# Performance work log

Measured on AMD Instinct MI355X. Metric: run time of the kernel, lower is better.

## Reference

```python
import jax, jax.numpy as jnp
import numpy as np

N_NODES = 100_000
N_EDGES = 1_600_000
N_GRAPHS = 512
HID = 64
NUM_CLASSES = 100
VOCAB = 3100
ID_OFFSET = 1500
BN_EPS = 1e-5


def setup_inputs() -> dict:
    key = jax.random.key(0)
    ks = jax.random.split(key, 8)
    node_ids = jax.random.randint(ks[0], (N_NODES,), 0, 1600)
    edge_src = jax.random.randint(ks[1], (N_EDGES,), 0, N_NODES)
    edge_dst = jax.random.randint(ks[2], (N_EDGES,), 0, N_NODES)
    graph_ids = jnp.sort(jax.random.randint(ks[3], (N_NODES,), 0, N_GRAPHS))
    emb = jax.random.normal(ks[4], (VOCAB, HID), dtype=jnp.float32) * 0.02
    # 3 GIN layers x 3 MLP linear layers, all 64->64 since embedding_dim == hidden
    Ws = jax.random.normal(ks[5], (3, 3, HID, HID), dtype=jnp.float32) * 0.05
    bs = jnp.zeros((3, 3, HID), dtype=jnp.float32)
    bn_gamma = jnp.ones((3, HID), dtype=jnp.float32)
    bn_beta = jnp.zeros((3, HID), dtype=jnp.float32)
    eps = jnp.zeros((3,), dtype=jnp.float32)  # learn_eps=True, init 0
    W_out = jax.random.normal(ks[6], (3 * HID, NUM_CLASSES), dtype=jnp.float32) * 0.05
    b_out = jnp.zeros((NUM_CLASSES,), dtype=jnp.float32)
    return {"node_ids": node_ids, "edge_src": edge_src, "edge_dst": edge_dst,
            "graph_ids": graph_ids, "emb": emb, "Ws": Ws, "bs": bs,
            "bn_gamma": bn_gamma, "bn_beta": bn_beta, "eps": eps,
            "W_out": W_out, "b_out": b_out}


def reference(node_ids, edge_src, edge_dst, graph_ids, emb, Ws, bs,
              bn_gamma, bn_beta, eps, W_out, b_out):
    n = node_ids.shape[0]
    h = emb[node_ids + ID_OFFSET]  # [N, HID]
    pooled = []
    for l in range(3):  # GIN layers (fixed small count)
        # GINConv, sum aggregator: (1+eps)*h + sum over in-edges of h[src]
        agg = jax.ops.segment_sum(h[edge_src], edge_dst, num_segments=n)
        x = (1.0 + eps[l]) * h + agg
        for m in range(3):
            x = jax.nn.relu(x @ Ws[l, m] + bs[l, m])
        mean = x.mean(axis=0)
        var = x.var(axis=0)  # biased var, as torch BN uses for normalization
        x = (x - mean) * jax.lax.rsqrt(var + BN_EPS) * bn_gamma[l] + bn_beta[l]
        h = x
        # dgl.sum_nodes: per-graph segment sum
        pooled.append(jax.ops.segment_sum(h, graph_ids, num_segments=N_GRAPHS))
    graph_features = jnp.concatenate(pooled, axis=-1)  # [G, 3*HID]
    return graph_features @ W_out + b_out  # [G, NUM_CLASSES]
```

## Files before the change

### kernel.cpp

```cpp
#include <hip/hip_runtime.h>

#define N_NODES 100000
#define N_EDGES 1600000
#define N_GRAPHS 512
#define HID 64
#define NUM_CLASSES 100
#define ID_OFFSET 1500
#define BN_EPS 1e-5f
#define CAP 64
#define NBKT 256
#define BSHIFT 9
#define NUSED ((N_NODES + 511) >> 9)
#define BCAP 10240
#define CBLK 98
#define CHUNK 16384
#define WPBLK 5
#define EMBBLK ((N_NODES * 32 + 1023) / 1024)
#define DUMMY_ROW 100000

typedef __attribute__((ext_vector_type(8))) short short8;
typedef __attribute__((ext_vector_type(4))) float floatx4;

__device__ __forceinline__ float b2f(unsigned short u) {
    return __builtin_bit_cast(float, ((unsigned)u) << 16);
}
__device__ __forceinline__ unsigned short f2b(float f) {
    unsigned x = __builtin_bit_cast(unsigned, f);
    x += 0x7FFFu + ((x >> 16) & 1u);
    return (unsigned short)(x >> 16);
}

#define XSH(row, qq) ((((((row) >> 4) << 7) + ((qq) << 4) + (((row) & 15) ^ (qq))) * 8))


__global__ __launch_bounds__(1024) void prep_kernel(const int* __restrict__ src,
                                                    const int* __restrict__ dst,
                                                    int* __restrict__ cursor,
                                                    int* __restrict__ rec,
                                                    const float* __restrict__ Ws,
                                                    unsigned short* __restrict__ whi,
                                                    unsigned short* __restrict__ wlo,
                                                    const int* __restrict__ node_ids,
                                                    const int* __restrict__ gid,
                                                    const float* __restrict__ emb,
                                                    unsigned short* __restrict__ h,
                                                    unsigned short* __restrict__ xin,
                                                    int* __restrict__ gs,
                                                    int* __restrict__ ge) {
    __shared__ int hist[NBKT];
    __shared__ int base_s[NBKT];
    int t = threadIdx.x;
    int blk = blockIdx.x;

    if (blk < CBLK) {
        if (blk == 0 && t < 32) {
            ((unsigned*)(h + (size_t)DUMMY_ROW * 64))[t] = 0u;
            ((unsigned*)(xin + (size_t)DUMMY_ROW * 64))[t] = 0u;
        }
        if (t < NBKT) hist[t] = 0;
        __syncthreads();
        int cb = blk * CHUNK;
        int d_[16], s_[16];
#pragma unroll
        for (int k = 0; k < 16; ++k) {
            int i = cb + k * 1024 + t;
            d_[k] = (i < N_EDGES) ? dst[i] : -1;
            s_[k] = (i < N_EDGES) ? src[i] : 0;
            if (d_[k] >= 0) atomicAdd(&hist[((unsigned)d_[k] >> BSHIFT) & (NBKT - 1)], 1);
        }
        __syncthreads();
        if (t < NBKT) base_s[t] = (hist[t] > 0) ? atomicAdd(&cursor[t], hist[t]) : 0;
        __syncthreads();
        if (t < NBKT) hist[t] = 0;
        __syncthreads();
#pragma unroll
        for (int k = 0; k < 16; ++k) {
            if (d_[k] >= 0) {
                unsigned d = (unsigned)d_[k];
                int b = (d >> BSHIFT) & (NBKT - 1);
                int p = atomicAdd(&hist[b], 1);
                int g = base_s[b] + p;
                if ((unsigned)g < BCAP)
                    rec[b * BCAP + g] = ((int)(d & 511) << 17) | (s_[k] & 0x1FFFF);
            }
        }
    } else if (blk < CBLK + WPBLK) {
        int G = (blk - CBLK) * 1024 + t;
        if (G < 3 * 1536) {
            int l = G / 1536, Gp = G % 1536;
            int mm = Gp >> 9, rem = Gp & 511;
            int kq = rem >> 6, n = rem & 63;
            const float* Wp = Ws + l * 12288 + mm * 4096 + (kq * 8) * 64 + n;
            unsigned short uh[8], ul[8];
#pragma unroll
            for (int j = 0; j < 8; ++j) {
                float w = Wp[j * 64];
                unsigned short hi = f2b(w);
                uh[j] = hi;
                ul[j] = f2b(w - b2f(hi));
            }
            size_t off = (size_t)l * 12288 + (mm << 12) + XSH(n, kq);
            *(short8*)&whi[off] = *(short8*)uh;
            *(short8*)&wlo[off] = *(short8*)ul;
        }
    } else {
        int idx = (blk - CBLK - WPBLK) * 1024 + t;
        if (idx < N_NODES * 32) {
            int n = idx >> 5, cp = idx & 31;
            const float2 e = *(const float2*)(emb + (((size_t)(node_ids[n] + ID_OFFSET)) << 6) + cp * 2);
            unsigned v = (unsigned)f2b(e.x) | ((unsigned)f2b(e.y) << 16);
            ((unsigned*)h)[n * 32 + cp] = v;
            if (cp == 0) {
                int g = gid[n] & (N_GRAPHS - 1);
                if (n == 0 || (gid[n - 1] & (N_GRAPHS - 1)) != g) gs[g] = n;
                if (n == N_NODES - 1 || (gid[n + 1] & (N_GRAPHS - 1)) != g) ge[g] = n + 1;
            }
        }
    }
}


__global__ __launch_bounds__(1024) void fill_kernel(const int* __restrict__ rec,
                                                    const int* __restrict__ cursor,
                                                    int* __restrict__ cnt,
                                                    int* __restrict__ srcs) {
    __shared__ int lcnt[512];
    int t = threadIdx.x;
    int b = blockIdx.x;
    if (t < 512) lcnt[t] = 0;
    __syncthreads();
    int nb = cursor[b];
    if (nb < 0) nb = 0;
    if (nb > BCAP) nb = BCAP;
    const int* seg = rec + b * BCAP;
    for (int i = t; i < nb; i += 1024) {
        unsigned r = (unsigned)seg[i];
        int dl = (int)((r >> 17) & 511);
        int s = (int)(r & 0x1FFFF);
        int node = (b << BSHIFT) + dl;
        int p = atomicAdd(&lcnt[dl], 1);
        if (p < CAP && node < N_NODES) srcs[(node << 6) + p] = s;
    }
    __syncthreads();
    if (t < 512) {
        int node = (b << BSHIFT) + t;
        if (node < N_NODES) {
            int deg = lcnt[t];
            cnt[node] = deg;
            int degc = deg > CAP ? CAP : deg;
            int degp = (degc + 15) & ~15;
            if (degp < 16) degp = 16;
            for (int p = degc; p < degp; ++p) srcs[(node << 6) + p] = DUMMY_ROW;
        }
    }
}


__global__ __launch_bounds__(256, 4) void fused_kernel(const unsigned short* __restrict__ x,
                                                       unsigned short* __restrict__ xo,
                                                       const int* __restrict__ cnt,
                                                       const int* __restrict__ srcs,
                                                       const float* __restrict__ eps, int l,
                                                       float* __restrict__ stats,
                                                       const float* __restrict__ gamma,
                                                       const float* __restrict__ beta,
                                                       const unsigned short* __restrict__ whi,
                                                       const unsigned short* __restrict__ wlo,
                                                       const float* __restrict__ bs,
                                                       const int* __restrict__ graph_ids,
                                                       float* __restrict__ pooled, int last) {
    __shared__ __align__(16) unsigned short xs[64 * 64];
    __shared__ int garr[64];
    __shared__ float ssum[256], sqq[256];
    int t = threadIdx.x;
    int nodebase = blockIdx.x * 64;
    int lane = t & 63, w = t >> 6;
    int half = lane >> 5, cl = lane & 31;
    const unsigned* __restrict__ xu = (const unsigned*)x;

    if (lane < 16) {
        int n = nodebase + w * 16 + lane;
        garr[w * 16 + lane] = (n < N_NODES) ? (graph_ids[n] & (N_GRAPHS - 1)) : -1;
    }

    float scale = 1.0f + eps[l];
    float a0f = 1.0f, a1f = 1.0f, b0f = 0.0f, b1f = 0.0f;
    if (l > 0) {
        int lp = l - 1;
        float2 sm = *(const float2*)&stats[lp * 128 + 2 * cl];
        float2 sq = *(const float2*)&stats[lp * 128 + 64 + 2 * cl];
        float2 gm = *(const float2*)&gamma[lp * 64 + 2 * cl];
        float2 bt = *(const float2*)&beta[lp * 64 + 2 * cl];
        float mean0 = sm.x * (1.0f / N_NODES);
        float var0 = sq.x * (1.0f / N_NODES) - mean0 * mean0;
        float r0 = rsqrtf(var0 + BN_EPS);
        a0f = gm.x * r0;
        b0f = bt.x - mean0 * a0f;
        float mean1 = sm.y * (1.0f / N_NODES);
        float var1 = sq.y * (1.0f / N_NODES) - mean1 * mean1;
        float r1 = rsqrtf(var1 + BN_EPS);
        a1f = gm.y * r1;
        b1f = bt.y - mean1 * a1f;
    }

    int wb = __builtin_amdgcn_readfirstlane(nodebase + w * 16);

    for (int g4 = 0; g4 < 4; ++g4) {
        int nb = wb + g4 * 4;
        int deg[4], degp[4];
        const int* row[4];
#pragma unroll
        for (int n = 0; n < 4; ++n) {
            int d = (nb + n < N_NODES) ? cnt[nb + n] : 0;
            int dc = d < 0 ? 0 : (d > CAP ? CAP : d);
            deg[n] = dc;
            int dp = (dc + 15) & ~15;
            degp[n] = dp < 16 ? 16 : dp;
            row[n] = srcs + ((size_t)(nb + n) << 6);
        }
        int cmax = degp[0];
        cmax = degp[1] > cmax ? degp[1] : cmax;
        cmax = degp[2] > cmax ? degp[2] : cmax;
        cmax = degp[3] > cmax ? degp[3] : cmax;

        unsigned us[4];
#pragma unroll
        for (int n = 0; n < 4; ++n) us[n] = xu[(size_t)(nb + n) * 32 + cl];

        float A0[4] = {0.f, 0.f, 0.f, 0.f}, A1[4] = {0.f, 0.f, 0.f, 0.f};
        float B0[4] = {0.f, 0.f, 0.f, 0.f}, B1[4] = {0.f, 0.f, 0.f, 0.f};

        {
            unsigned uv[4][8];
#pragma unroll
            for (int n = 0; n < 4; ++n)
#pragma unroll
                for (int k = 0; k < 8; ++k) {
                    int ia = row[n][2 * k] & 0x1FFFF;
                    int ib = row[n][2 * k + 1] & 0x1FFFF;
                    int idx = half ? ib : ia;
                    uv[n][k] = xu[(size_t)idx * 32 + cl];
                }
#pragma unroll
            for (int n = 0; n < 4; ++n)
#pragma unroll
                for (int k = 0; k < 8; ++k) {
                    float lo = b2f((unsigned short)(uv[n][k] & 0xFFFF));
                    float hi = b2f((unsigned short)(uv[n][k] >> 16));
                    if (k & 1) { B0[n] += lo; B1[n] += hi; }
                    else       { A0[n] += lo; A1[n] += hi; }
                }
        }
        for (int c = 16; c < cmax; c += 16) {
            unsigned uc[4][8];
#pragma unroll
            for (int n = 0; n < 4; ++n)
                if (c < degp[n])
#pragma unroll
                    for (int k = 0; k < 8; ++k) {
                        int ia = row[n][c + 2 * k] & 0x1FFFF;
                        int ib = row[n][c + 2 * k + 1] & 0x1FFFF;
                        int idx = half ? ib : ia;
                        uc[n][k] = xu[(size_t)idx * 32 + cl];
                    }
#pragma unroll
            for (int n = 0; n < 4; ++n)
                if (c < degp[n])
#pragma unroll
                    for (int k = 0; k < 8; ++k) {
                        float lo = b2f((unsigned short)(uc[n][k] & 0xFFFF));
                        float hi = b2f((unsigned short)(uc[n][k] >> 16));
                        if (k & 1) { B0[n] += lo; B1[n] += hi; }
                        else       { A0[n] += lo; A1[n] += hi; }
                    }
        }

#pragma unroll
        for (int n = 0; n < 4; ++n) {
            float S0 = A0[n] + B0[n];
            float S1 = A1[n] + B1[n];
            S0 += __shfl_xor(S0, 32);
            S1 += __shfl_xor(S1, 32);
            if (half == 0) {
                float selflo = b2f((unsigned short)(us[n] & 0xFFFF));
                float selfhi = b2f((unsigned short)(us[n] >> 16));
                float db = scale + (float)deg[n];
                float v0 = fmaf(a0f, fmaf(scale, selflo, S0), db * b0f);
                float v1 = fmaf(a1f, fmaf(scale, selfhi, S1), db * b1f);
                int r = w * 16 + g4 * 4 + n;
                int col = 2 * cl;
                *(unsigned*)&xs[XSH(r, col >> 3) + (col & 7)] =
                    (unsigned)f2b(v0) | ((unsigned)f2b(v1) << 16);
            }
        }
    }

    int m = lane & 15, q = lane >> 4;
    const float* bb = bs + l * 3 * 64;
    const unsigned short* whil = whi + (size_t)l * 12288;
    const unsigned short* wlol = wlo + (size_t)l * 12288;
    for (int mm = 0; mm < 3; ++mm) {
        short8 bl[2][4];
#pragma unroll
        for (int kc = 0; kc < 2; ++kc)
#pragma unroll
            for (int tj = 0; tj < 4; ++tj)
                bl[kc][tj] = *(const short8*)&wlol[(mm << 12) + XSH(tj * 16 + m, kc * 4 + q)];
        short8 a[2];
#pragma unroll
        for (int kc = 0; kc < 2; ++kc)
            a[kc] = *(const short8*)&xs[XSH(w * 16 + m, kc * 4 + q)];

        floatx4 acc[4];
#pragma unroll
        for (int tj = 0; tj < 4; ++tj) {
            float bv = bb[mm * 64 + tj * 16 + m];
            acc[tj] = (floatx4){bv, bv, bv, bv};
        }
#pragma unroll
        for (int kc = 0; kc < 2; ++kc) {
            short8 bh[4];
#pragma unroll
            for (int tj = 0; tj < 4; ++tj)
                bh[tj] = *(const short8*)&whil[(mm << 12) + XSH(tj * 16 + m, kc * 4 + q)];
#pragma unroll
            for (int tj = 0; tj < 4; ++tj)
                acc[tj] = __builtin_amdgcn_mfma_f32_16x16x32_bf16(a[kc], bh[tj], acc[tj], 0, 0, 0);
        }
#pragma unroll
        for (int kc = 0; kc < 2; ++kc)
#pragma unroll
            for (int tj = 0; tj < 4; ++tj)
                acc[tj] = __builtin_amdgcn_mfma_f32_16x16x32_bf16(a[kc], bl[kc][tj], acc[tj], 0, 0, 0);
#pragma unroll
        for (int tj = 0; tj < 4; ++tj) {
            int col = tj * 16 + m;
#pragma unroll
            for (int r = 0; r < 4; ++r) {
                int row = w * 16 + q * 4 + r;
                float v = acc[tj][r];
                xs[XSH(row, col >> 3) + (col & 7)] = f2b(v > 0.f ? v : 0.f);
            }
        }
    }

    if (!last) {
        unsigned* xou = (unsigned*)xo;
#pragma unroll
        for (int it = 0; it < 8; ++it) {
            int row = w * 16 + (lane >> 5) + it * 2;
            int cp = lane & 31;
            int col = cp * 2;
            unsigned val = *(const unsigned*)&xs[XSH(row, col >> 3) + (col & 7)];
            int node = nodebase + row;
            if (node < N_NODES) xou[(size_t)node * 32 + cp] = val;
        }
    }
    {
        int c = lane;
        float s = 0.f, q2 = 0.f, acc2 = 0.f;
        int cur = -1;
        for (int k = 0; k < 16; ++k) {
            int row = w * 16 + k;
            int g = garr[row];
            if (g >= 0) {
                float v = b2f(xs[XSH(row, c >> 3) + (c & 7)]);
                s += v;
                q2 += v * v;
                if (g != cur) {
                    if (cur >= 0) atomicAdd(&pooled[cur * 192 + l * 64 + c], acc2);
                    acc2 = 0.f;
                    cur = g;
                }
                acc2 += v;
            }
        }
        if (cur >= 0) atomicAdd(&pooled[cur * 192 + l * 64 + c], acc2);
        ssum[t] = s;
        sqq[t] = q2;
    }
    __syncthreads();
    if (t < 64) {
        float S = ssum[t] + ssum[t + 64] + ssum[t + 128] + ssum[t + 192];
        float Q = sqq[t] + sqq[t + 64] + sqq[t + 128] + sqq[t + 192];
        atomicAdd(&stats[l * 128 + t], S);
        atomicAdd(&stats[l * 128 + 64 + t], Q);
    }
}


__global__ __launch_bounds__(256) void out_kernel(const float* __restrict__ pooled,
                                                  const float* __restrict__ stats,
                                                  const float* __restrict__ gamma,
                                                  const float* __restrict__ beta,
                                                  const int* __restrict__ gs,
                                                  const int* __restrict__ ge,
                                                  const float* __restrict__ Wo,
                                                  const float* __restrict__ bo,
                                                  float* __restrict__ out) {
    __shared__ float sab[384];
    int t = threadIdx.x;
    if (t < 192) {
        int l2 = t / 64, c = t & 63;
        float mean = stats[l2 * 128 + c] * (1.0f / N_NODES);
        float var = stats[l2 * 128 + 64 + c] * (1.0f / N_NODES) - mean * mean;
        float rstd = rsqrtf(var + BN_EPS);
        float a = gamma[l2 * 64 + c] * rstd;
        sab[l2 * 128 + c] = a;
        sab[l2 * 128 + 64 + c] = beta[l2 * 64 + c] - mean * a;
    }
    __syncthreads();
    int idx = blockIdx.x * blockDim.x + t;
    if (idx < N_GRAPHS * NUM_CLASSES) {
        int g = idx / NUM_CLASSES, k = idx % NUM_CLASSES;
        float cg = (float)(ge[g] - gs[g]);
        float acc = bo[k];
        for (int l2 = 0; l2 < 3; ++l2)
            for (int c = 0; c < 64; ++c) {
                float gf = fmaf(sab[l2 * 128 + c], pooled[g * 192 + l2 * 64 + c],
                                sab[l2 * 128 + 64 + c] * cg);
                acc = fmaf(gf, Wo[(l2 * 64 + c) * NUM_CLASSES + k], acc);
            }
        out[idx] = acc;
    }
}

extern "C" void kernel_launch(void* const* d_in, const int* in_sizes, int n_in,
                              void* d_out, int out_size, void* d_ws, size_t ws_size,
                              hipStream_t stream) {
    const int*   node_ids  = (const int*)d_in[0];
    const int*   edge_src  = (const int*)d_in[1];
    const int*   edge_dst  = (const int*)d_in[2];
    const int*   graph_ids = (const int*)d_in[3];
    const float* emb       = (const float*)d_in[4];
    const float* Ws        = (const float*)d_in[5];
    const float* bs        = (const float*)d_in[6];
    const float* gamma     = (const float*)d_in[7];
    const float* beta      = (const float*)d_in[8];
    const float* eps       = (const float*)d_in[9];
    const float* W_out     = (const float*)d_in[10];
    const float* b_out     = (const float*)d_in[11];
    float* out = (float*)d_out;

    unsigned short* h    = (unsigned short*)d_ws;
    unsigned short* xin  = h + 6400000 + 8192;
    unsigned short* whi  = xin + 6400000 + 8192;
    unsigned short* wlo  = whi + 36864;
    int*   srcs   = (int*)(wlo + 36864);
    int*   rec    = srcs + 6400000;
    float* pooled = (float*)(rec + NUSED * BCAP);
    float* stats  = pooled + 98304;
    int*   cnt    = (int*)(stats + 384);
    int*   gs     = cnt + 100000;
    int*   ge     = gs + 512;
    int*   cursor = ge + 512;

    hipMemsetAsync(pooled, 0,
                   (size_t)(98304 + 384 + 100000 + 512 + 512 + 256) * 4, stream);

    prep_kernel<<<CBLK + WPBLK + EMBBLK, 1024, 0, stream>>>(
        edge_src, edge_dst, cursor, rec, Ws, whi, wlo,
        node_ids, graph_ids, emb, h, xin, gs, ge);
    fill_kernel<<<NUSED, 1024, 0, stream>>>(rec, cursor, cnt, srcs);

    const int FUSE_BLK = (N_NODES + 63) / 64;
    for (int l = 0; l < 3; ++l) {
        const unsigned short* X = (l % 2 == 0) ? h : xin;
        unsigned short* A = (l % 2 == 0) ? xin : h;
        fused_kernel<<<FUSE_BLK, 256, 0, stream>>>(
            X, A, cnt, srcs, eps, l, stats, gamma, beta,
            whi, wlo, bs, graph_ids, pooled, l == 2);
    }

    out_kernel<<<(N_GRAPHS * NUM_CLASSES + 255) / 256, 256, 0, stream>>>(
        pooled, stats, gamma, beta, gs, ge, W_out, b_out, out);
}
```

Measured before the change: 344.7 us.

## Split fused GIN layer into separate aggregation and MLP kernels, replicate BN stats

Splits the per-layer fused gather+MLP kernel into an aggregation kernel (4 nodes per wave, no LDS, finer-grained blocks) and an MLP kernel that reloads the aggregated rows from global memory in place. BN statistic atomics are spread over 8 replicated slots to reduce contention, and readers sum the replicas. The fill kernel's dummy padding is parallelised across all threads. The split adds an extra global write and read of the node features per layer in exchange for higher occupancy during the latency-bound gather.

```diff
diff --git a/kernel.cpp b/kernel.cpp
--- a/kernel.cpp
+++ b/kernel.cpp
@@ -17,6 +17,8 @@
 #define WPBLK 5
 #define EMBBLK ((N_NODES * 32 + 1023) / 1024)
 #define DUMMY_ROW 100000
+#define SREP 8
+#define SSTRIDE 384
 
 typedef __attribute__((ext_vector_type(8))) short short8;
 typedef __attribute__((ext_vector_type(4))) float floatx4;
@@ -144,155 +146,177 @@
     __syncthreads();
     if (t < 512) {
         int node = (b << BSHIFT) + t;
+        if (node < N_NODES) cnt[node] = lcnt[t];
+    }
+    __syncthreads();
+    for (int i = t; i < 512 * 64; i += 1024) {
+        int nl = i >> 6, p = i & 63;
+        int node = (b << BSHIFT) + nl;
         if (node < N_NODES) {
-            int deg = lcnt[t];
-            cnt[node] = deg;
+            int deg = lcnt[nl];
             int degc = deg > CAP ? CAP : deg;
             int degp = (degc + 15) & ~15;
             if (degp < 16) degp = 16;
-            for (int p = degc; p < degp; ++p) srcs[(node << 6) + p] = DUMMY_ROW;
-        }
-    }
-}
-
-
-__global__ __launch_bounds__(256, 4) void fused_kernel(const unsigned short* __restrict__ x,
-                                                       unsigned short* __restrict__ xo,
-                                                       const int* __restrict__ cnt,
-                                                       const int* __restrict__ srcs,
-                                                       const float* __restrict__ eps, int l,
-                                                       float* __restrict__ stats,
-                                                       const float* __restrict__ gamma,
-                                                       const float* __restrict__ beta,
-                                                       const unsigned short* __restrict__ whi,
-                                                       const unsigned short* __restrict__ wlo,
-                                                       const float* __restrict__ bs,
-                                                       const int* __restrict__ graph_ids,
-                                                       float* __restrict__ pooled, int last) {
+            if (p >= degc && p < degp) srcs[(node << 6) + p] = DUMMY_ROW;
+        }
+    }
+}
+
+
+__global__ __launch_bounds__(256) void agg_kernel(const unsigned short* __restrict__ x,
+                                                  const int* __restrict__ cnt,
+                                                  const int* __restrict__ srcs,
+                                                  const float* __restrict__ eps, int l,
+                                                  const float* __restrict__ stats,
+                                                  const float* __restrict__ gamma,
+                                                  const float* __restrict__ beta,
+                                                  unsigned short* __restrict__ out) {
+    int nb = __builtin_amdgcn_readfirstlane(((blockIdx.x << 2) + (threadIdx.x >> 6)) << 2);
+    int lane = threadIdx.x & 63;
+    int half = lane >> 5;
+    int cl = lane & 31;
+    const unsigned* __restrict__ xu = (const unsigned*)x;
+
+    float scale = 1.0f + eps[l];
+    float a0f = 1.0f, a1f = 1.0f, b0f = 0.0f, b1f = 0.0f;
+    if (l > 0) {
+        int lp = l - 1;
+        float sm0 = 0.f, sm1 = 0.f, sq0 = 0.f, sq1 = 0.f;
+#pragma unroll
+        for (int rp = 0; rp < SREP; ++rp) {
+            const float* sp = stats + rp * SSTRIDE + lp * 128;
+            float2 a_ = *(const float2*)&sp[2 * cl];
+            float2 b_ = *(const float2*)&sp[64 + 2 * cl];
+            sm0 += a_.x; sm1 += a_.y;
+            sq0 += b_.x; sq1 += b_.y;
+        }
+        float2 gm = *(const float2*)&gamma[lp * 64 + 2 * cl];
+        float2 bt = *(const float2*)&beta[lp * 64 + 2 * cl];
+        float mean0 = sm0 * (1.0f / N_NODES);
+        float var0 = sq0 * (1.0f / N_NODES) - mean0 * mean0;
+        float r0 = rsqrtf(var0 + BN_EPS);
+        a0f = gm.x * r0;
+        b0f = bt.x - mean0 * a0f;
+        float mean1 = sm1 * (1.0f / N_NODES);
+        float var1 = sq1 * (1.0f / N_NODES) - mean1 * mean1;
+        float r1 = rsqrtf(var1 + BN_EPS);
+        a1f = gm.y * r1;
+        b1f = bt.y - mean1 * a1f;
+    }
+
+    int deg[4], degp[4];
+    const int* row[4];
+#pragma unroll
+    for (int n = 0; n < 4; ++n) {
+        int d = cnt[nb + n];
+        int dc = d < 0 ? 0 : (d > CAP ? CAP : d);
+        deg[n] = dc;
+        int dp = (dc + 15) & ~15;
+        degp[n] = dp < 16 ? 16 : dp;
+        row[n] = srcs + ((size_t)(nb + n) << 6);
+    }
+    int cmax = degp[0];
+    cmax = degp[1] > cmax ? degp[1] : cmax;
+    cmax = degp[2] > cmax ? degp[2] : cmax;
+    cmax = degp[3] > cmax ? degp[3] : cmax;
+
+    unsigned us[4];
+#pragma unroll
+    for (int n = 0; n < 4; ++n) us[n] = xu[(size_t)(nb + n) * 32 + cl];
+
+    float A0[4] = {0.f, 0.f, 0.f, 0.f}, A1[4] = {0.f, 0.f, 0.f, 0.f};
+    float B0[4] = {0.f, 0.f, 0.f, 0.f}, B1[4] = {0.f, 0.f, 0.f, 0.f};
+
+    {
+        unsigned uv[4][8];
+#pragma unroll
+        for (int n = 0; n < 4; ++n)
+#pragma unroll
+            for (int k = 0; k < 8; ++k) {
+                int ia = row[n][2 * k] & 0x1FFFF;
+                int ib = row[n][2 * k + 1] & 0x1FFFF;
+                int idx = half ? ib : ia;
+                uv[n][k] = xu[(size_t)idx * 32 + cl];
+            }
+#pragma unroll
+        for (int n = 0; n < 4; ++n)
+#pragma unroll
+            for (int k = 0; k < 8; ++k) {
+                float lo = b2f((unsigned short)(uv[n][k] & 0xFFFF));
+                float hi = b2f((unsigned short)(uv[n][k] >> 16));
+                if (k & 1) { B0[n] += lo; B1[n] += hi; }
+                else       { A0[n] += lo; A1[n] += hi; }
+            }
+    }
+
+    for (int c = 16; c < cmax; c += 16) {
+        unsigned uc[4][8];
+#pragma unroll
+        for (int n = 0; n < 4; ++n)
+            if (c < degp[n])
+#pragma unroll
+                for (int k = 0; k < 8; ++k) {
+                    int ia = row[n][c + 2 * k] & 0x1FFFF;
+                    int ib = row[n][c + 2 * k + 1] & 0x1FFFF;
+                    int idx = half ? ib : ia;
+                    uc[n][k] = xu[(size_t)idx * 32 + cl];
+                }
+#pragma unroll
+        for (int n = 0; n < 4; ++n)
+            if (c < degp[n])
+#pragma unroll
+                for (int k = 0; k < 8; ++k) {
+                    float lo = b2f((unsigned short)(uc[n][k] & 0xFFFF));
+                    float hi = b2f((unsigned short)(uc[n][k] >> 16));
+                    if (k & 1) { B0[n] += lo; B1[n] += hi; }
+                    else       { A0[n] += lo; A1[n] += hi; }
+                }
+    }
+
+#pragma unroll
+    for (int n = 0; n < 4; ++n) {
+        float S0 = (A0[n] + B0[n]);
+        float S1 = (A1[n] + B1[n]);
+        S0 += __shfl_xor(S0, 32);
+        S1 += __shfl_xor(S1, 32);
+        if (half == 0) {
+            float selflo = b2f((unsigned short)(us[n] & 0xFFFF));
+            float selfhi = b2f((unsigned short)(us[n] >> 16));
+            float db = scale + (float)deg[n];
+            float v0 = fmaf(a0f, fmaf(scale, selflo, S0), db * b0f);
+            float v1 = fmaf(a1f, fmaf(scale, selfhi, S1), db * b1f);
+            ((unsigned*)out)[(size_t)(nb + n) * 32 + cl] =
+                (unsigned)f2b(v0) | ((unsigned)f2b(v1) << 16);
+        }
+    }
+}
+
+
+__global__ __launch_bounds__(256, 4) void mlp_kernel(unsigned short* __restrict__ x,
+                                                     const unsigned short* __restrict__ whi,
+                                                     const unsigned short* __restrict__ wlo,
+                                                     const float* __restrict__ bs, int l,
+                                                     float* __restrict__ stats,
+                                                     const int* __restrict__ graph_ids,
+                                                     float* __restrict__ pooled, int last) {
     __shared__ __align__(16) unsigned short xs[64 * 64];
     __shared__ int garr[64];
     __shared__ float ssum[256], sqq[256];
     int t = threadIdx.x;
     int nodebase = blockIdx.x * 64;
     int lane = t & 63, w = t >> 6;
-    int half = lane >> 5, cl = lane & 31;
-    const unsigned* __restrict__ xu = (const unsigned*)x;
 
     if (lane < 16) {
         int n = nodebase + w * 16 + lane;
         garr[w * 16 + lane] = (n < N_NODES) ? (graph_ids[n] & (N_GRAPHS - 1)) : -1;
     }
-
-    float scale = 1.0f + eps[l];
-    float a0f = 1.0f, a1f = 1.0f, b0f = 0.0f, b1f = 0.0f;
-    if (l > 0) {
-        int lp = l - 1;
-        float2 sm = *(const float2*)&stats[lp * 128 + 2 * cl];
-        float2 sq = *(const float2*)&stats[lp * 128 + 64 + 2 * cl];
-        float2 gm = *(const float2*)&gamma[lp * 64 + 2 * cl];
-        float2 bt = *(const float2*)&beta[lp * 64 + 2 * cl];
-        float mean0 = sm.x * (1.0f / N_NODES);
-        float var0 = sq.x * (1.0f / N_NODES) - mean0 * mean0;
-        float r0 = rsqrtf(var0 + BN_EPS);
-        a0f = gm.x * r0;
-        b0f = bt.x - mean0 * a0f;
-        float mean1 = sm.y * (1.0f / N_NODES);
-        float var1 = sq.y * (1.0f / N_NODES) - mean1 * mean1;
-        float r1 = rsqrtf(var1 + BN_EPS);
-        a1f = gm.y * r1;
-        b1f = bt.y - mean1 * a1f;
-    }
-
-    int wb = __builtin_amdgcn_readfirstlane(nodebase + w * 16);
-
-    for (int g4 = 0; g4 < 4; ++g4) {
-        int nb = wb + g4 * 4;
-        int deg[4], degp[4];
-        const int* row[4];
-#pragma unroll
-        for (int n = 0; n < 4; ++n) {
-            int d = (nb + n < N_NODES) ? cnt[nb + n] : 0;
-            int dc = d < 0 ? 0 : (d > CAP ? CAP : d);
-            deg[n] = dc;
-            int dp = (dc + 15) & ~15;
-            degp[n] = dp < 16 ? 16 : dp;
-            row[n] = srcs + ((size_t)(nb + n) << 6);
-        }
-        int cmax = degp[0];
-        cmax = degp[1] > cmax ? degp[1] : cmax;
-        cmax = degp[2] > cmax ? degp[2] : cmax;
-        cmax = degp[3] > cmax ? degp[3] : cmax;
-
-        unsigned us[4];
-#pragma unroll
-        for (int n = 0; n < 4; ++n) us[n] = xu[(size_t)(nb + n) * 32 + cl];
-
-        float A0[4] = {0.f, 0.f, 0.f, 0.f}, A1[4] = {0.f, 0.f, 0.f, 0.f};
-        float B0[4] = {0.f, 0.f, 0.f, 0.f}, B1[4] = {0.f, 0.f, 0.f, 0.f};
-
-        {
-            unsigned uv[4][8];
-#pragma unroll
-            for (int n = 0; n < 4; ++n)
-#pragma unroll
-                for (int k = 0; k < 8; ++k) {
-                    int ia = row[n][2 * k] & 0x1FFFF;
-                    int ib = row[n][2 * k + 1] & 0x1FFFF;
-                    int idx = half ? ib : ia;
-                    uv[n][k] = xu[(size_t)idx * 32 + cl];
-                }
-#pragma unroll
-            for (int n = 0; n < 4; ++n)
-#pragma unroll
-                for (int k = 0; k < 8; ++k) {
-                    float lo = b2f((unsigned short)(uv[n][k] & 0xFFFF));
-                    float hi = b2f((unsigned short)(uv[n][k] >> 16));
-                    if (k & 1) { B0[n] += lo; B1[n] += hi; }
-                    else       { A0[n] += lo; A1[n] += hi; }
-                }
-        }
-        for (int c = 16; c < cmax; c += 16) {
-            unsigned uc[4][8];
-#pragma unroll
-            for (int n = 0; n < 4; ++n)
-                if (c < degp[n])
-#pragma unroll
-                    for (int k = 0; k < 8; ++k) {
-                        int ia = row[n][c + 2 * k] & 0x1FFFF;
-                        int ib = row[n][c + 2 * k + 1] & 0x1FFFF;
-                        int idx = half ? ib : ia;
-                        uc[n][k] = xu[(size_t)idx * 32 + cl];
-                    }
-#pragma unroll
-            for (int n = 0; n < 4; ++n)
-                if (c < degp[n])
-#pragma unroll
-                    for (int k = 0; k < 8; ++k) {
-                        float lo = b2f((unsigned short)(uc[n][k] & 0xFFFF));
-                        float hi = b2f((unsigned short)(uc[n][k] >> 16));
-                        if (k & 1) { B0[n] += lo; B1[n] += hi; }
-                        else       { A0[n] += lo; A1[n] += hi; }
-                    }
-        }
-
-#pragma unroll
-        for (int n = 0; n < 4; ++n) {
-            float S0 = A0[n] + B0[n];
-            float S1 = A1[n] + B1[n];
-            S0 += __shfl_xor(S0, 32);
-            S1 += __shfl_xor(S1, 32);
-            if (half == 0) {
-                float selflo = b2f((unsigned short)(us[n] & 0xFFFF));
-                float selfhi = b2f((unsigned short)(us[n] >> 16));
-                float db = scale + (float)deg[n];
-                float v0 = fmaf(a0f, fmaf(scale, selflo, S0), db * b0f);
-                float v1 = fmaf(a1f, fmaf(scale, selfhi, S1), db * b1f);
-                int r = w * 16 + g4 * 4 + n;
-                int col = 2 * cl;
-                *(unsigned*)&xs[XSH(r, col >> 3) + (col & 7)] =
-                    (unsigned)f2b(v0) | ((unsigned)f2b(v1) << 16);
-            }
-        }
+#pragma unroll
+    for (int i = 0; i < 2; ++i) {
+        int g = i * 64 + lane;
+        int rl = g >> 3, qr = g & 7;
+        int row = w * 16 + rl;
+        const int4 v = *(const int4*)(x + (((size_t)(nodebase + row)) << 6) + qr * 8);
+        *(int4*)&xs[XSH(row, qr)] = v;
     }
 
     int m = lane & 15, q = lane >> 4;
@@ -345,7 +369,7 @@
     }
 
     if (!last) {
-        unsigned* xou = (unsigned*)xo;
+        unsigned* xo = (unsigned*)x;
 #pragma unroll
         for (int it = 0; it < 8; ++it) {
             int row = w * 16 + (lane >> 5) + it * 2;
@@ -353,13 +377,14 @@
             int col = cp * 2;
             unsigned val = *(const unsigned*)&xs[XSH(row, col >> 3) + (col & 7)];
             int node = nodebase + row;
-            if (node < N_NODES) xou[(size_t)node * 32 + cp] = val;
+            if (node < N_NODES) xo[(size_t)node * 32 + cp] = val;
         }
     }
     {
         int c = lane;
         float s = 0.f, q2 = 0.f, acc2 = 0.f;
         int cur = -1;
+#pragma unroll
         for (int k = 0; k < 16; ++k) {
             int row = w * 16 + k;
             int g = garr[row];
@@ -383,8 +408,9 @@
     if (t < 64) {
         float S = ssum[t] + ssum[t + 64] + ssum[t + 128] + ssum[t + 192];
         float Q = sqq[t] + sqq[t + 64] + sqq[t + 128] + sqq[t + 192];
-        atomicAdd(&stats[l * 128 + t], S);
-        atomicAdd(&stats[l * 128 + 64 + t], Q);
+        float* sp = stats + (blockIdx.x & (SREP - 1)) * SSTRIDE + l * 128;
+        atomicAdd(&sp[t], S);
+        atomicAdd(&sp[64 + t], Q);
     }
 }
 
@@ -402,8 +428,14 @@
     int t = threadIdx.x;
     if (t < 192) {
         int l2 = t / 64, c = t & 63;
-        float mean = stats[l2 * 128 + c] * (1.0f / N_NODES);
-        float var = stats[l2 * 128 + 64 + c] * (1.0f / N_NODES) - mean * mean;
+        float S = 0.f, Q = 0.f;
+#pragma unroll
+        for (int rp = 0; rp < SREP; ++rp) {
+            S += stats[rp * SSTRIDE + l2 * 128 + c];
+            Q += stats[rp * SSTRIDE + l2 * 128 + 64 + c];
+        }
+        float mean = S * (1.0f / N_NODES);
+        float var = Q * (1.0f / N_NODES) - mean * mean;
         float rstd = rsqrtf(var + BN_EPS);
         float a = gamma[l2 * 64 + c] * rstd;
         sab[l2 * 128 + c] = a;
@@ -450,26 +482,26 @@
     int*   rec    = srcs + 6400000;
     float* pooled = (float*)(rec + NUSED * BCAP);
     float* stats  = pooled + 98304;
-    int*   cnt    = (int*)(stats + 384);
+    int*   cnt    = (int*)(stats + SREP * SSTRIDE);
     int*   gs     = cnt + 100000;
     int*   ge     = gs + 512;
     int*   cursor = ge + 512;
 
     hipMemsetAsync(pooled, 0,
-                   (size_t)(98304 + 384 + 100000 + 512 + 512 + 256) * 4, stream);
+                   (size_t)(98304 + SREP * SSTRIDE + 100000 + 512 + 512 + 256) * 4, stream);
 
     prep_kernel<<<CBLK + WPBLK + EMBBLK, 1024, 0, stream>>>(
         edge_src, edge_dst, cursor, rec, Ws, whi, wlo,
         node_ids, graph_ids, emb, h, xin, gs, ge);
     fill_kernel<<<NUSED, 1024, 0, stream>>>(rec, cursor, cnt, srcs);
 
-    const int FUSE_BLK = (N_NODES + 63) / 64;
+    const int MLP_BLK = (N_NODES + 63) / 64;
+    const int AGG_BLK = N_NODES / 16;
     for (int l = 0; l < 3; ++l) {
-        const unsigned short* X = (l % 2 == 0) ? h : xin;
+        unsigned short* X = (l % 2 == 0) ? h : xin;
         unsigned short* A = (l % 2 == 0) ? xin : h;
-        fused_kernel<<<FUSE_BLK, 256, 0, stream>>>(
-            X, A, cnt, srcs, eps, l, stats, gamma, beta,
-            whi, wlo, bs, graph_ids, pooled, l == 2);
+        agg_kernel<<<AGG_BLK, 256, 0, stream>>>(X, cnt, srcs, eps, l, stats, gamma, beta, A);
+        mlp_kernel<<<MLP_BLK, 256, 0, stream>>>(A, whi, wlo, bs, l, stats, graph_ids, pooled, l == 2);
     }
 
     out_kernel<<<(N_GRAPHS * NUM_CLASSES + 255) / 256, 256, 0, stream>>>(
```

Measured after the change: 299.7 us. -13.1%, faster.
